# Kernel optimization log

Hardware: AMD Instinct MI355X
Metric: run time of the kernel (lower is better)

Reference implementation:

```python
import jax, jax.numpy as jnp
import numpy as np

B, D, N, M, R, C = 512, 16, 64, 32, 32, 10  # batch, divisions, feat_in, feat_map, TR-rank, categories


def setup_inputs() -> dict:
    key = jax.random.key(0)
    k1, k2, k3, k4 = jax.random.split(key, 4)
    tensor = jax.random.normal(k1, (B, D, N), dtype=jnp.float32)
    W_fm = jax.random.normal(k2, (N, M), dtype=jnp.float32) / np.sqrt(N)
    b_fm = jax.random.normal(k3, (M,), dtype=jnp.float32) * 0.01
    # one [R, M, R] tensor-ring core per (category, division)
    G = jax.random.normal(k4, (C, D, R, M, R), dtype=jnp.float32) / np.sqrt(M * R)
    return {"tensor": tensor, "W_fm": W_fm, "b_fm": b_fm, "G": G}


def reference(tensor, W_fm, b_fm, G):
    # FeatureMap: learned linear n -> m applied per division  [B, D, M]
    feat = jnp.einsum('bdn,nm->bdm', tensor, W_fm) + b_fm
    # CoreKernelTensorRing per (category, division): [B,M] x [R,M,R] -> [B,R,R]
    cores = jnp.einsum('bdm,cdimj->cdbij', feat, G)  # [C, D, B, R, R]
    # __foward_products: chained batched matmul along divisions (structural loop, D fixed)
    prod = cores[:, 0]  # [C, B, R, R]
    for d in range(1, D):
        prod = jnp.matmul(prod, cores[:, d])
    # __calculate_traces: per-sample trace, one logit per category
    logits = jnp.einsum('cbii->bc', prod)  # [B, C]
    return jax.nn.log_softmax(logits, axis=1)
```

## Files before the change

### kernel.cpp

```cpp
#include <hip/hip_runtime.h>
#include <math.h>

#define BB 512
#define DD 16
#define NN 64
#define MM 32
#define RR 32
#define CC 10
#define ISTR 40
#define BSTR 1288

typedef _Float16 v8h __attribute__((ext_vector_type(8)));
typedef float v4f __attribute__((ext_vector_type(4)));
typedef float v16f __attribute__((ext_vector_type(16)));

union H8 { unsigned int u[4]; v8h h; _Float16 e[8]; };
union H4 { unsigned int u[2]; _Float16 e[4]; };

__device__ inline unsigned pk2(float a, float b) {
    union { unsigned u; _Float16 e[2]; } v;
    v.e[0] = (_Float16)a; v.e[1] = (_Float16)b;
    return v.u;
}

__global__ __launch_bounds__(256) void produce_kernel(
    const float* __restrict__ tensor, const float* __restrict__ W,
    const float* __restrict__ bias,   const float* __restrict__ G,
    _Float16* __restrict__ fh,        _Float16* __restrict__ gh) {
    __shared__ __align__(16) char smem[36864];
    const int t = threadIdx.x;
    if (blockIdx.x < 1024) {
        float* ten_s = (float*)smem;
        float* W_s   = (float*)smem + 512;
        const int bd0 = blockIdx.x * 8;
        if (t < 128)
            *(float4*)(ten_s + t * 4) = *(const float4*)(tensor + bd0 * NN + t * 4);
        *(float4*)(W_s + t * 4)        = *(const float4*)(W + t * 4);
        *(float4*)(W_s + 1024 + t * 4) = *(const float4*)(W + 1024 + t * 4);
        __syncthreads();
        const int m = t & 31, bd_l = t >> 5;
        float acc = bias[m];
#pragma unroll
        for (int n = 0; n < NN; ++n) acc += ten_s[bd_l * NN + n] * W_s[n * MM + m];
        fh[(bd0 + bd_l) * MM + m] = (_Float16)acc;
    } else {
        _Float16* lg = (_Float16*)smem;
        const int pb = blockIdx.x - 1024;
        const int c  = pb >> 5;
        const int d  = (pb >> 1) & 15;
        const int hf = pb & 1;
        const float* src = G + (size_t)(c * DD + d) * 32768 + hf * 16384;
#pragma unroll
        for (int k = 0; k < 16; ++k) {
            const int f = (k * 256 + t) * 4;
            float4 v = *(const float4*)(src + f);
            const int di = f >> 10, m = (f >> 5) & 31, j = f & 31;
            H4 hv;
            hv.e[0] = (_Float16)v.x; hv.e[1] = (_Float16)v.y;
            hv.e[2] = (_Float16)v.z; hv.e[3] = (_Float16)v.w;
            *(uint2*)(lg + di * 1152 + m * 36 + j) = make_uint2(hv.u[0], hv.u[1]);
        }
        __syncthreads();
#pragma unroll
        for (int k = 0; k < 8; ++k) {
            const int idx = k * 256 + t;
            const int tl = idx >> 6, ln = idx & 63;
            const int di = tl >> 1, ks = tl & 1;
            const int hh = ln >> 5, j = ln & 31;
            H8 o;
#pragma unroll
            for (int r = 0; r < 8; ++r)
                o.e[r] = lg[di * 1152 + (16 * ks + 8 * hh + r) * 36 + j];
            const size_t gi = ((size_t)(c * DD + d) * 64 + hf * 32 + tl) * 64 + ln;
            *(v8h*)(gh + gi * 8) = o.h;
        }
    }
}

__global__ __launch_bounds__(512, 2) void chain_kernel(
    const _Float16* __restrict__ feat_h,
    const _Float16* __restrict__ g_h,
    float* __restrict__ trout)
{
    __shared__ __align__(16) _Float16 lds[32 * BSTR];

    const int bid = blockIdx.x;
    const int xcd = bid & 7;
    const int idx = bid >> 3;
    int c, sub;
    if (idx < 16) { c = xcd; sub = idx; }
    else {
        const int e = idx - 16;
        c = 8 + (xcd >> 2);
        sub = (xcd & 3) * 4 + e;
    }
    const int b0 = sub * 32;
    const int t    = threadIdx.x;
    const int w    = t >> 6;
    const int lane = t & 63;
    const int h    = lane >> 5;
    const int col  = lane & 31;

    const size_t gc = (size_t)c * DD * 32768;
    const _Float16* fb = feat_h + (size_t)(b0 + col) * (DD * MM);

    const v16f z16 = {0.f,0.f,0.f,0.f,0.f,0.f,0.f,0.f,
                      0.f,0.f,0.f,0.f,0.f,0.f,0.f,0.f};

    v8h af[2];
#pragma unroll
    for (int ks = 0; ks < 2; ++ks)
        af[ks] = *(const v8h*)(fb + 16 * ks + 8 * h);
    v8h gB[4][2];
#pragma unroll
    for (int il = 0; il < 4; ++il)
#pragma unroll
        for (int ks = 0; ks < 2; ++ks)
            gB[il][ks] = *(const v8h*)(g_h + gc +
                ((size_t)(((4 * w + il) * 2 + ks) * 64) + lane) * 8);

    v8h sb[4][2];

    for (int d = 0; d < DD; ++d) {
        __syncthreads();
        v16f av[4];
#pragma unroll
        for (int il = 0; il < 4; ++il) {
            av[il] = __builtin_amdgcn_mfma_f32_32x32x16_f16(af[0], gB[il][0], z16, 0, 0, 0);
            av[il] = __builtin_amdgcn_mfma_f32_32x32x16_f16(af[1], gB[il][1], av[il], 0, 0, 0);
        }
        if (d < DD - 1) {
#pragma unroll
            for (int ks = 0; ks < 2; ++ks)
                af[ks] = *(const v8h*)(fb + (d + 1) * MM + 16 * ks + 8 * h);
            const size_t gb = gc + (size_t)(d + 1) * 32768;
#pragma unroll
            for (int il = 0; il < 4; ++il)
#pragma unroll
                for (int ks = 0; ks < 2; ++ks)
                    gB[il][ks] = *(const v8h*)(g_h + gb +
                        ((size_t)(((4 * w + il) * 2 + ks) * 64) + lane) * 8);
        }
#pragma unroll
        for (int r16 = 0; r16 < 16; ++r16) {
            const int b = (r16 & 3) + 8 * (r16 >> 2) + 4 * h;
            H4 hv;
            hv.e[0] = (_Float16)av[0][r16];
            hv.e[1] = (_Float16)av[1][r16];
            hv.e[2] = (_Float16)av[2][r16];
            hv.e[3] = (_Float16)av[3][r16];
            *(uint2*)(lds + b * BSTR + col * ISTR + 4 * w) =
                make_uint2(hv.u[0], hv.u[1]);
        }
        __syncthreads();
#pragma unroll
        for (int cc = 0; cc < 4; ++cc) {
            _Float16* base = lds + (4 * w + cc) * BSTR;
            if (d == 0) {
#pragma unroll
                for (int ks = 0; ks < 2; ++ks) {
                    H8 x;
#pragma unroll
                    for (int r = 0; r < 8; ++r)
                        x.e[r] = base[(16 * ks + 8 * h + r) * ISTR + col];
                    sb[cc][ks] = x.h;
                }
            } else {
                v8h a0 = *(const v8h*)(base + col * ISTR + 8 * h);
                v8h a1 = *(const v8h*)(base + col * ISTR + 16 + 8 * h);
                v16f acc;
                acc = __builtin_amdgcn_mfma_f32_32x32x16_f16(a0, sb[cc][0], z16, 0, 0, 0);
                acc = __builtin_amdgcn_mfma_f32_32x32x16_f16(a1, sb[cc][1], acc, 0, 0, 0);
                if (d == DD - 1) {
                    float ts = 0.f;
#pragma unroll
                    for (int r16 = 0; r16 < 16; ++r16) {
                        const int row = (r16 & 3) + 8 * (r16 >> 2) + 4 * h;
                        if (row == col) ts += acc[r16];
                    }
#pragma unroll
                    for (int off = 32; off > 0; off >>= 1)
                        ts += __shfl_xor(ts, off);
                    if (lane == 0)
                        trout[(size_t)(b0 + 4 * w + cc) * CC + c] = ts;
                } else {
                    const unsigned A0 = pk2(acc[0],  acc[1]);
                    const unsigned A1 = pk2(acc[2],  acc[3]);
                    const unsigned B0 = pk2(acc[4],  acc[5]);
                    const unsigned B1 = pk2(acc[6],  acc[7]);
                    const unsigned C0 = pk2(acc[8],  acc[9]);
                    const unsigned C1 = pk2(acc[10], acc[11]);
                    const unsigned D0 = pk2(acc[12], acc[13]);
                    const unsigned D1 = pk2(acc[14], acc[15]);
                    const unsigned pA0 = (unsigned)__shfl_xor((int)A0, 32);
                    const unsigned pA1 = (unsigned)__shfl_xor((int)A1, 32);
                    const unsigned pB0 = (unsigned)__shfl_xor((int)B0, 32);
                    const unsigned pB1 = (unsigned)__shfl_xor((int)B1, 32);
                    const unsigned pC0 = (unsigned)__shfl_xor((int)C0, 32);
                    const unsigned pC1 = (unsigned)__shfl_xor((int)C1, 32);
                    const unsigned pD0 = (unsigned)__shfl_xor((int)D0, 32);
                    const unsigned pD1 = (unsigned)__shfl_xor((int)D1, 32);
                    H8 s0, s1;
                    s0.u[0] = h ? pB0 : A0;  s0.u[1] = h ? pB1 : A1;
                    s0.u[2] = h ? B0 : pA0;  s0.u[3] = h ? B1 : pA1;
                    s1.u[0] = h ? pD0 : C0;  s1.u[1] = h ? pD1 : C1;
                    s1.u[2] = h ? D0 : pC0;  s1.u[3] = h ? D1 : pC1;
                    sb[cc][0] = s0.h;
                    sb[cc][1] = s1.h;
                }
            }
        }
    }
}

__global__ __launch_bounds__(256) void lsm_kernel(
    const float* __restrict__ tr, float* __restrict__ out) {
    const int b = blockIdx.x * 256 + threadIdx.x;
    float v[CC];
    float mx = -1e30f;
#pragma unroll
    for (int c = 0; c < CC; ++c) {
        v[c] = tr[b * CC + c];
        mx = fmaxf(mx, v[c]);
    }
    float ssum = 0.f;
#pragma unroll
    for (int c = 0; c < CC; ++c) ssum += expf(v[c] - mx);
    const float ls = logf(ssum);
#pragma unroll
    for (int c = 0; c < CC; ++c) out[b * CC + c] = v[c] - mx - ls;
}

extern "C" void kernel_launch(void* const* d_in, const int* in_sizes, int n_in,
                              void* d_out, int out_size, void* d_ws, size_t ws_size,
                              hipStream_t stream) {
    const float* tensor = (const float*)d_in[0];
    const float* W      = (const float*)d_in[1];
    const float* bias   = (const float*)d_in[2];
    const float* G      = (const float*)d_in[3];
    float* out = (float*)d_out;

    const size_t FEAT = (size_t)BB * DD * MM;
    const size_t GPK  = (size_t)CC * DD * 64 * 64 * 8;
    _Float16* fh = (_Float16*)d_ws;
    _Float16* gh = fh + FEAT;
    float* trbuf = (float*)(gh + GPK);

    produce_kernel<<<1024 + 320, 256, 0, stream>>>(tensor, W, bias, G, fh, gh);
    chain_kernel<<<160, 512, 0, stream>>>(fh, gh, trbuf);
    lsm_kernel<<<BB / 256, 256, 0, stream>>>(trbuf, out);
}
```

Measured before the change: 120.4 us.

## Permute inner rank index to drop cross-lane shuffles in chained product

Applies a fixed permutation to the contracted rank index when writing cores to LDS, so the MFMA accumulator layout can be fed back directly as the next B operand without the xor-32 shuffle exchange. The d==0 special-case gather from LDS is replaced by an identity matrix seeded in registers, so every division runs the same MFMA path. This removes 8 shuffles and selects per step, plus the strided scalar LDS gather, at the cost of one extra MFMA pair at d=0. The trace is invariant under the permutation as long as it is applied consistently to the contracted index.

```diff
diff --git a/kernel.cpp b/kernel.cpp
--- a/kernel.cpp
+++ b/kernel.cpp
@@ -101,6 +101,8 @@
     const int h    = lane >> 5;
     const int col  = lane & 31;
 
+    const int wp4 = 4 * ((w & 4) | ((w & 1) << 1) | ((w & 2) >> 1));
+
     const size_t gc = (size_t)c * DD * 32768;
     const _Float16* fb = feat_h + (size_t)(b0 + col) * (DD * MM);
 
@@ -120,6 +122,17 @@
                 ((size_t)(((4 * w + il) * 2 + ks) * 64) + lane) * 8);
 
     v8h sb[4][2];
+    {
+        H8 x0, x1;
+#pragma unroll
+        for (int r = 0; r < 8; ++r) {
+            const int pi = (r & 3) + 8 * (r >> 2) + 4 * h;
+            x0.e[r] = (_Float16)((pi == col) ? 1.0f : 0.0f);
+            x1.e[r] = (_Float16)((pi + 16 == col) ? 1.0f : 0.0f);
+        }
+#pragma unroll
+        for (int cc = 0; cc < 4; ++cc) { sb[cc][0] = x0.h; sb[cc][1] = x1.h; }
+    }
 
     for (int d = 0; d < DD; ++d) {
         __syncthreads();
@@ -149,65 +162,42 @@
             hv.e[1] = (_Float16)av[1][r16];
             hv.e[2] = (_Float16)av[2][r16];
             hv.e[3] = (_Float16)av[3][r16];
-            *(uint2*)(lds + b * BSTR + col * ISTR + 4 * w) =
+            *(uint2*)(lds + b * BSTR + col * ISTR + wp4) =
                 make_uint2(hv.u[0], hv.u[1]);
         }
         __syncthreads();
 #pragma unroll
         for (int cc = 0; cc < 4; ++cc) {
             _Float16* base = lds + (4 * w + cc) * BSTR;
-            if (d == 0) {
-#pragma unroll
-                for (int ks = 0; ks < 2; ++ks) {
-                    H8 x;
-#pragma unroll
-                    for (int r = 0; r < 8; ++r)
-                        x.e[r] = base[(16 * ks + 8 * h + r) * ISTR + col];
-                    sb[cc][ks] = x.h;
+            v8h a0 = *(const v8h*)(base + col * ISTR + 8 * h);
+            v8h a1 = *(const v8h*)(base + col * ISTR + 16 + 8 * h);
+            v16f acc;
+            acc = __builtin_amdgcn_mfma_f32_32x32x16_f16(a0, sb[cc][0], z16, 0, 0, 0);
+            acc = __builtin_amdgcn_mfma_f32_32x32x16_f16(a1, sb[cc][1], acc, 0, 0, 0);
+            if (d == DD - 1) {
+                float ts = 0.f;
+#pragma unroll
+                for (int r16 = 0; r16 < 16; ++r16) {
+                    const int row = (r16 & 3) + 8 * (r16 >> 2) + 4 * h;
+                    if (row == col) ts += acc[r16];
                 }
+#pragma unroll
+                for (int off = 32; off > 0; off >>= 1)
+                    ts += __shfl_xor(ts, off);
+                if (lane == 0)
+                    trout[(size_t)(b0 + 4 * w + cc) * CC + c] = ts;
             } else {
-                v8h a0 = *(const v8h*)(base + col * ISTR + 8 * h);
-                v8h a1 = *(const v8h*)(base + col * ISTR + 16 + 8 * h);
-                v16f acc;
-                acc = __builtin_amdgcn_mfma_f32_32x32x16_f16(a0, sb[cc][0], z16, 0, 0, 0);
-                acc = __builtin_amdgcn_mfma_f32_32x32x16_f16(a1, sb[cc][1], acc, 0, 0, 0);
-                if (d == DD - 1) {
-                    float ts = 0.f;
-#pragma unroll
-                    for (int r16 = 0; r16 < 16; ++r16) {
-                        const int row = (r16 & 3) + 8 * (r16 >> 2) + 4 * h;
-                        if (row == col) ts += acc[r16];
-                    }
-#pragma unroll
-                    for (int off = 32; off > 0; off >>= 1)
-                        ts += __shfl_xor(ts, off);
-                    if (lane == 0)
-                        trout[(size_t)(b0 + 4 * w + cc) * CC + c] = ts;
-                } else {
-                    const unsigned A0 = pk2(acc[0],  acc[1]);
-                    const unsigned A1 = pk2(acc[2],  acc[3]);
-                    const unsigned B0 = pk2(acc[4],  acc[5]);
-                    const unsigned B1 = pk2(acc[6],  acc[7]);
-                    const unsigned C0 = pk2(acc[8],  acc[9]);
-                    const unsigned C1 = pk2(acc[10], acc[11]);
-                    const unsigned D0 = pk2(acc[12], acc[13]);
-                    const unsigned D1 = pk2(acc[14], acc[15]);
-                    const unsigned pA0 = (unsigned)__shfl_xor((int)A0, 32);
-                    const unsigned pA1 = (unsigned)__shfl_xor((int)A1, 32);
-                    const unsigned pB0 = (unsigned)__shfl_xor((int)B0, 32);
-                    const unsigned pB1 = (unsigned)__shfl_xor((int)B1, 32);
-                    const unsigned pC0 = (unsigned)__shfl_xor((int)C0, 32);
-                    const unsigned pC1 = (unsigned)__shfl_xor((int)C1, 32);
-                    const unsigned pD0 = (unsigned)__shfl_xor((int)D0, 32);
-                    const unsigned pD1 = (unsigned)__shfl_xor((int)D1, 32);
-                    H8 s0, s1;
-                    s0.u[0] = h ? pB0 : A0;  s0.u[1] = h ? pB1 : A1;
-                    s0.u[2] = h ? B0 : pA0;  s0.u[3] = h ? B1 : pA1;
-                    s1.u[0] = h ? pD0 : C0;  s1.u[1] = h ? pD1 : C1;
-                    s1.u[2] = h ? D0 : pC0;  s1.u[3] = h ? D1 : pC1;
-                    sb[cc][0] = s0.h;
-                    sb[cc][1] = s1.h;
-                }
+                H8 s0, s1;
+                s0.u[0] = pk2(acc[0],  acc[1]);
+                s0.u[1] = pk2(acc[2],  acc[3]);
+                s0.u[2] = pk2(acc[4],  acc[5]);
+                s0.u[3] = pk2(acc[6],  acc[7]);
+                s1.u[0] = pk2(acc[8],  acc[9]);
+                s1.u[1] = pk2(acc[10], acc[11]);
+                s1.u[2] = pk2(acc[12], acc[13]);
+                s1.u[3] = pk2(acc[14], acc[15]);
+                sb[cc][0] = s0.h;
+                sb[cc][1] = s1.h;
             }
         }
     }
```

Measured after the change: 116.6 us. -3.2%, faster.
